# Kernel tuning notes

Hardware: AMD Instinct MI355X
Metric: run time of the kernel (lower is better)

Reference implementation:

```python
import jax, jax.numpy as jnp
import numpy as np

N = 200000          # nodes
E = 12_800_000      # edges (avg degree 64)
C = 4               # conv_out_channels == node_features
H = 32              # lstm_out_channels


def setup_inputs() -> dict:
    key = jax.random.key(0)
    ks = jax.random.split(key, 16)
    inv_c = 1.0 / np.sqrt(C)
    inv_h = 1.0 / np.sqrt(H)
    return {
        "x": jax.random.normal(ks[0], (N, C), jnp.float32),
        "edge_index": jax.random.randint(ks[1], (2, E), 0, N, dtype=jnp.int64),
        "edge_weight": jax.random.uniform(ks[2], (E,), jnp.float32),
        "h_0": 0.1 * jax.random.normal(ks[3], (1, N, H), jnp.float32),
        "c_0": 0.1 * jax.random.normal(ks[4], (1, N, H), jnp.float32),
        # GatedGraphConv (num_layers=1): weight[0] of shape [C, C]
        "conv_weight": inv_c * jax.random.normal(ks[5], (C, C), jnp.float32),
        # GRUCell(C, C) params (PyTorch layout: [3C, C], gate order r,z,n)
        "gru_w_ih": inv_c * jax.random.normal(ks[6], (3 * C, C), jnp.float32),
        "gru_w_hh": inv_c * jax.random.normal(ks[7], (3 * C, C), jnp.float32),
        "gru_b_ih": inv_c * jax.random.normal(ks[8], (3 * C,), jnp.float32),
        "gru_b_hh": inv_c * jax.random.normal(ks[9], (3 * C,), jnp.float32),
        # LSTM(C, H, 1 layer) params (PyTorch layout: [4H, *], gate order i,f,g,o)
        "lstm_w_ih": inv_h * jax.random.normal(ks[10], (4 * H, C), jnp.float32),
        "lstm_w_hh": inv_h * jax.random.normal(ks[11], (4 * H, H), jnp.float32),
        "lstm_b_ih": inv_h * jax.random.normal(ks[12], (4 * H,), jnp.float32),
        "lstm_b_hh": inv_h * jax.random.normal(ks[13], (4 * H,), jnp.float32),
        # Linear(32, 1)
        "lin_w": inv_h * jax.random.normal(ks[14], (1, H), jnp.float32),
        "lin_b": inv_h * jax.random.normal(ks[15], (1,), jnp.float32),
    }


def reference(x, edge_index, edge_weight, h_0, c_0,
              conv_weight, gru_w_ih, gru_w_hh, gru_b_ih, gru_b_hh,
              lstm_w_ih, lstm_w_hh, lstm_b_ih, lstm_b_hh, lin_w, lin_b):
    n = x.shape[0]
    src, dst = edge_index[0], edge_index[1]  # source j -> target i

    # ---- GatedGraphConv, 1 layer (in_dim == out_channels, no padding) ----
    m = x @ conv_weight                                   # [N, C]
    msg = m[src] * edge_weight[:, None]                   # [E, C] gather
    summed = jax.ops.segment_sum(msg, dst, num_segments=n)
    cnt = jax.ops.segment_sum(jnp.ones((msg.shape[0],), msg.dtype), dst,
                              num_segments=n)
    agg = summed / jnp.maximum(cnt, 1.0)[:, None]         # mean aggr (empty -> 0)

    # GRUCell(agg, x): r,z,n gate order
    gi = agg @ gru_w_ih.T + gru_b_ih
    gh = x @ gru_w_hh.T + gru_b_hh
    i_r, i_z, i_n = jnp.split(gi, 3, axis=1)
    h_r, h_z, h_n = jnp.split(gh, 3, axis=1)
    r = jax.nn.sigmoid(i_r + h_r)
    z = jax.nn.sigmoid(i_z + h_z)
    nn_ = jnp.tanh(i_n + r * h_n)
    h_conv = (1.0 - z) * nn_ + z * x                      # [N, C]

    # ---- LSTM: seq_len=1, batch=N, 1 layer; gate order i,f,g,o ----
    h_prev, c_prev = h_0[0], c_0[0]                       # [N, H]
    gates = h_conv @ lstm_w_ih.T + lstm_b_ih + h_prev @ lstm_w_hh.T + lstm_b_hh
    ig, fg, gg, og = jnp.split(gates, 4, axis=1)
    ig, fg, og = jax.nn.sigmoid(ig), jax.nn.sigmoid(fg), jax.nn.sigmoid(og)
    gg = jnp.tanh(gg)
    c_new = fg * c_prev + ig * gg
    h_new = og * jnp.tanh(c_new)                          # [N, H]

    # ---- relu + linear head ----
    out = jax.nn.relu(h_new) @ lin_w.T + lin_b            # [N, 1]
    return out, h_new[None], c_new[None]
```

## Files before the change

### kernel.cpp

```cpp
#include <hip/hip_runtime.h>
#include <math.h>

#define B_SHIFT 8
#define BMASK   255
#define CHUNK   8192
#define CITER   (CHUNK / (NTHR * 4))
#define NTHR    256
#define SEG     4

#define LDSADD(p, v) __hip_atomic_fetch_add((p), (v), __ATOMIC_RELAXED, \
                                            __HIP_MEMORY_SCOPE_WORKGROUP)

static __device__ __forceinline__ float sigf(float x) {
  return 1.0f / (1.0f + __expf(-x));
}
static __device__ __forceinline__ float tanhfast(float x) {
  return 2.0f / (1.0f + __expf(-2.0f * x)) - 1.0f;
}

__global__ void conv_m_kernel(const float* __restrict__ x,
                              const float* __restrict__ w,
                              float* __restrict__ m, int n) {
  int i = blockIdx.x * blockDim.x + threadIdx.x;
  if (i >= n) return;
  float4 xv = reinterpret_cast<const float4*>(x)[i];
  float4 mv;
  mv.x = xv.x * w[0] + xv.y * w[4] + xv.z * w[8]  + xv.w * w[12];
  mv.y = xv.x * w[1] + xv.y * w[5] + xv.z * w[9]  + xv.w * w[13];
  mv.z = xv.x * w[2] + xv.y * w[6] + xv.z * w[10] + xv.w * w[14];
  mv.w = xv.x * w[3] + xv.y * w[7] + xv.z * w[11] + xv.w * w[15];
  reinterpret_cast<float4*>(m)[i] = mv;
}


__global__ __launch_bounds__(NTHR) void hist_kernel(const int* __restrict__ dst,
                                                    int E, int B,
                                                    int* __restrict__ gCnt) {
  __shared__ int h[1024];
  for (int b = threadIdx.x; b < B; b += NTHR) h[b] = 0;
  __syncthreads();
  const int4* d4 = reinterpret_cast<const int4*>(dst);
  int i4base = (int)(((long long)blockIdx.x * CHUNK) >> 2);
  int lim4 = E >> 2;
#pragma unroll
  for (int j = 0; j < CITER; ++j) {
    int i4 = i4base + j * NTHR + threadIdx.x;
    if (i4 < lim4) {
      int4 d = d4[i4];
      atomicAdd(&h[d.x >> B_SHIFT], 1);
      atomicAdd(&h[d.y >> B_SHIFT], 1);
      atomicAdd(&h[d.z >> B_SHIFT], 1);
      atomicAdd(&h[d.w >> B_SHIFT], 1);
    }
  }
  if (blockIdx.x == 0 && threadIdx.x == 0) {
    for (int e = E & ~3; e < E; ++e) atomicAdd(&h[dst[e] >> B_SHIFT], 1);
  }
  __syncthreads();
  for (int b = threadIdx.x; b < B; b += NTHR) {
    int c = h[b];
    if (c) atomicAdd(&gCnt[b], c);
  }
}

__global__ void scan_kernel(const int* __restrict__ gCnt, int B,
                            int* __restrict__ start, int* __restrict__ cursor) {
  __shared__ int s[1024];
  int t = threadIdx.x;
  int v = (t < B) ? gCnt[t] : 0;
  s[t] = v;
  __syncthreads();
  for (int off = 1; off < 1024; off <<= 1) {
    int u = (t >= off) ? s[t - off] : 0;
    __syncthreads();
    s[t] += u;
    __syncthreads();
  }
  if (t < B) {
    int excl = (t == 0) ? 0 : s[t - 1];
    start[t] = excl;
    cursor[t] = excl;
  }
  if (t == 0) start[B] = s[1023];
}

__global__ __launch_bounds__(NTHR) void bin_kernel(const int* __restrict__ ei,
                                                   const float* __restrict__ ew,
                                                   int E, int B,
                                                   int* __restrict__ cursor,
                                                   int2* __restrict__ binned) {
  __shared__ int h[1024];
  for (int b = threadIdx.x; b < B; b += NTHR) h[b] = 0;
  __syncthreads();
  const int* dst = ei + E;
  const int4* d4 = reinterpret_cast<const int4*>(dst);
  const int4* s4 = reinterpret_cast<const int4*>(ei);
  const float4* w4 = reinterpret_cast<const float4*>(ew);
  int i4base = (int)(((long long)blockIdx.x * CHUNK) >> 2);
  int lim4 = E >> 2;
#pragma unroll
  for (int j = 0; j < CITER; ++j) {
    int i4 = i4base + j * NTHR + threadIdx.x;
    if (i4 < lim4) {
      int4 d = d4[i4];
      atomicAdd(&h[d.x >> B_SHIFT], 1);
      atomicAdd(&h[d.y >> B_SHIFT], 1);
      atomicAdd(&h[d.z >> B_SHIFT], 1);
      atomicAdd(&h[d.w >> B_SHIFT], 1);
    }
  }
  __syncthreads();
  for (int b = threadIdx.x; b < B; b += NTHR) {
    int c = h[b];
    if (c) h[b] = atomicAdd(&cursor[b], c);
  }
  __syncthreads();
#pragma unroll
  for (int j = 0; j < CITER; ++j) {
    int i4 = i4base + j * NTHR + threadIdx.x;
    if (i4 < lim4) {
      int4 d = d4[i4];
      int4 s = s4[i4];
      float4 w = w4[i4];
      int p;
      p = atomicAdd(&h[d.x >> B_SHIFT], 1);
      binned[p] = make_int2((s.x << B_SHIFT) | (d.x & BMASK), __float_as_int(w.x));
      p = atomicAdd(&h[d.y >> B_SHIFT], 1);
      binned[p] = make_int2((s.y << B_SHIFT) | (d.y & BMASK), __float_as_int(w.y));
      p = atomicAdd(&h[d.z >> B_SHIFT], 1);
      binned[p] = make_int2((s.z << B_SHIFT) | (d.z & BMASK), __float_as_int(w.z));
      p = atomicAdd(&h[d.w >> B_SHIFT], 1);
      binned[p] = make_int2((s.w << B_SHIFT) | (d.w & BMASK), __float_as_int(w.w));
    }
  }
  if (blockIdx.x == 0 && threadIdx.x == 0) {
    for (int e = E & ~3; e < E; ++e) {
      int d = dst[e];
      int p = atomicAdd(&cursor[d >> B_SHIFT], 1);
      binned[p] = make_int2((ei[e] << B_SHIFT) | (d & BMASK), __float_as_int(ew[e]));
    }
  }
}

__global__ __launch_bounds__(NTHR) void edge_agg_kernel(
    const float* __restrict__ m, const int2* __restrict__ binned,
    const int* __restrict__ start, float* __restrict__ sumBuf,
    float* __restrict__ cntBuf, int n) {
  __shared__ float acc[NTHR * 5];
  int tid = threadIdx.x;
  int b = blockIdx.x;
#pragma unroll
  for (int k = 0; k < 5; ++k) acc[k * NTHR + tid] = 0.0f;
  __syncthreads();

  int s0 = start[b], e0 = start[b + 1];
  int len = e0 - s0;
  int s = s0 + (int)((long long)len * blockIdx.y / SEG);
  int e = s0 + (int)((long long)len * (blockIdx.y + 1) / SEG);

  const float4* m4 = reinterpret_cast<const float4*>(m);
  int i = s + tid;
  for (; i + 7 * NTHR < e; i += 8 * NTHR) {
    int2 r[8];
    float4 v[8];
#pragma unroll
    for (int u = 0; u < 8; ++u) r[u] = binned[i + u * NTHR];
#pragma unroll
    for (int u = 0; u < 8; ++u) v[u] = m4[r[u].x >> B_SHIFT];
#pragma unroll
    for (int u = 0; u < 8; ++u) {
      float w = __int_as_float(r[u].y);
      int a = (r[u].x & BMASK) * 5;
      LDSADD(&acc[a + 0], v[u].x * w);
      LDSADD(&acc[a + 1], v[u].y * w);
      LDSADD(&acc[a + 2], v[u].z * w);
      LDSADD(&acc[a + 3], v[u].w * w);
      LDSADD(&acc[a + 4], 1.0f);
    }
  }
  for (; i < e; i += NTHR) {
    int2 r = binned[i];
    float4 v = m4[r.x >> B_SHIFT];
    float w = __int_as_float(r.y);
    int a = (r.x & BMASK) * 5;
    LDSADD(&acc[a + 0], v.x * w);
    LDSADD(&acc[a + 1], v.y * w);
    LDSADD(&acc[a + 2], v.z * w);
    LDSADD(&acc[a + 3], v.w * w);
    LDSADD(&acc[a + 4], 1.0f);
  }
  __syncthreads();

  int node = (b << B_SHIFT) + tid;
  if (node < n) {
    float c = acc[tid * 5 + 4];
    if (c != 0.0f) {
      unsafeAtomicAdd(&sumBuf[(size_t)node * 4 + 0], acc[tid * 5 + 0]);
      unsafeAtomicAdd(&sumBuf[(size_t)node * 4 + 1], acc[tid * 5 + 1]);
      unsafeAtomicAdd(&sumBuf[(size_t)node * 4 + 2], acc[tid * 5 + 2]);
      unsafeAtomicAdd(&sumBuf[(size_t)node * 4 + 3], acc[tid * 5 + 3]);
      unsafeAtomicAdd(&cntBuf[node], c);
    }
  }
}

__global__ __launch_bounds__(NTHR) void node_kernel2(
    const float* __restrict__ x, const float* __restrict__ sumBuf,
    const float* __restrict__ cntBuf,
    const float* __restrict__ h0, const float* __restrict__ c0,
    const float* __restrict__ gwi, const float* __restrict__ gwh,
    const float* __restrict__ gbi, const float* __restrict__ gbh,
    const float* __restrict__ lwi, const float* __restrict__ lwh,
    const float* __restrict__ lbi, const float* __restrict__ lbh,
    const float* __restrict__ linw, const float* __restrict__ linb,
    float* __restrict__ out, float* __restrict__ hout, float* __restrict__ cout,
    int n) {
  __shared__ float4 s_lwh[1024];
  __shared__ float4 s_lwi[128];
  __shared__ float  s_lb[128];
  __shared__ float  s_linw[32];
  __shared__ float  s_gwi[48], s_gwh[48], s_gbi[12], s_gbh[12];

  int tid = threadIdx.x;
  for (int k = tid; k < 4096; k += NTHR) ((float*)s_lwh)[k] = lwh[k];
  for (int k = tid; k < 512; k += NTHR) ((float*)s_lwi)[k] = lwi[k];
  if (tid < 128) s_lb[tid] = lbi[tid] + lbh[tid];
  if (tid < 32) s_linw[tid] = linw[tid];
  if (tid < 48) { s_gwi[tid] = gwi[tid]; s_gwh[tid] = gwh[tid]; }
  if (tid < 12) { s_gbi[tid] = gbi[tid]; s_gbh[tid] = gbh[tid]; }
  __syncthreads();

  int i = blockIdx.x * blockDim.x + tid;
  if (i >= n) return;

  float4 sv = reinterpret_cast<const float4*>(sumBuf)[i];
  float inv = 1.0f / fmaxf(cntBuf[i], 1.0f);
  float agg[4] = {sv.x * inv, sv.y * inv, sv.z * inv, sv.w * inv};
  float4 xv = reinterpret_cast<const float4*>(x)[i];
  float xa[4] = {xv.x, xv.y, xv.z, xv.w};

  float hc[4];
#pragma unroll
  for (int c = 0; c < 4; ++c) {
    float gi_r = s_gbi[c],     gh_r = s_gbh[c];
    float gi_z = s_gbi[4 + c], gh_z = s_gbh[4 + c];
    float gi_n = s_gbi[8 + c], gh_n = s_gbh[8 + c];
#pragma unroll
    for (int k = 0; k < 4; ++k) {
      gi_r += agg[k] * s_gwi[c * 4 + k];       gh_r += xa[k] * s_gwh[c * 4 + k];
      gi_z += agg[k] * s_gwi[(4 + c) * 4 + k]; gh_z += xa[k] * s_gwh[(4 + c) * 4 + k];
      gi_n += agg[k] * s_gwi[(8 + c) * 4 + k]; gh_n += xa[k] * s_gwh[(8 + c) * 4 + k];
    }
    float r = sigf(gi_r + gh_r);
    float z = sigf(gi_z + gh_z);
    float nn = tanhfast(gi_n + r * gh_n);
    hc[c] = (1.0f - z) * nn + z * xa[c];
  }

  const float4* h04 = reinterpret_cast<const float4*>(h0) + (size_t)i * 8;
  const float4* c04 = reinterpret_cast<const float4*>(c0) + (size_t)i * 8;
  float hp[32];
#pragma unroll
  for (int q = 0; q < 8; ++q) {
    float4 hv = h04[q];
    hp[q * 4 + 0] = hv.x; hp[q * 4 + 1] = hv.y;
    hp[q * 4 + 2] = hv.z; hp[q * 4 + 3] = hv.w;
  }
  float oacc = linb[0];
  float4* hout4 = reinterpret_cast<float4*>(hout) + (size_t)i * 8;
  float4* cout4 = reinterpret_cast<float4*>(cout) + (size_t)i * 8;

#pragma unroll
  for (int jc = 0; jc < 8; ++jc) {
    float4 cpv = c04[jc];
    float cpa[4] = {cpv.x, cpv.y, cpv.z, cpv.w};
    float hn[4], cn[4];
#pragma unroll
    for (int jj = 0; jj < 4; ++jj) {
      int j = jc * 4 + jj;
      float gI = s_lb[j];
      float gF = s_lb[32 + j];
      float gG = s_lb[64 + j];
      float gO = s_lb[96 + j];
      float4 wi = s_lwi[j], wf = s_lwi[32 + j], wg = s_lwi[64 + j], wo = s_lwi[96 + j];
      gI += hc[0] * wi.x + hc[1] * wi.y + hc[2] * wi.z + hc[3] * wi.w;
      gF += hc[0] * wf.x + hc[1] * wf.y + hc[2] * wf.z + hc[3] * wf.w;
      gG += hc[0] * wg.x + hc[1] * wg.y + hc[2] * wg.z + hc[3] * wg.w;
      gO += hc[0] * wo.x + hc[1] * wo.y + hc[2] * wo.z + hc[3] * wo.w;
#pragma unroll
      for (int q = 0; q < 8; ++q) {
        float4 a = s_lwh[j * 8 + q];
        float4 b = s_lwh[(32 + j) * 8 + q];
        float4 g = s_lwh[(64 + j) * 8 + q];
        float4 o = s_lwh[(96 + j) * 8 + q];
        float p0 = hp[q * 4 + 0], p1 = hp[q * 4 + 1];
        float p2 = hp[q * 4 + 2], p3 = hp[q * 4 + 3];
        gI += p0 * a.x + p1 * a.y + p2 * a.z + p3 * a.w;
        gF += p0 * b.x + p1 * b.y + p2 * b.z + p3 * b.w;
        gG += p0 * g.x + p1 * g.y + p2 * g.z + p3 * g.w;
        gO += p0 * o.x + p1 * o.y + p2 * o.z + p3 * o.w;
      }
      float ig = sigf(gI), fg = sigf(gF), og = sigf(gO), gg = tanhfast(gG);
      float cnew = fg * cpa[jj] + ig * gg;
      float hnew = og * tanhfast(cnew);
      cn[jj] = cnew; hn[jj] = hnew;
      oacc += fmaxf(hnew, 0.0f) * s_linw[j];
    }
    hout4[jc] = make_float4(hn[0], hn[1], hn[2], hn[3]);
    cout4[jc] = make_float4(cn[0], cn[1], cn[2], cn[3]);
  }
  out[i] = oacc;
}


__global__ void edge_kernel(const int* __restrict__ ei,
                            const float* __restrict__ ew,
                            const float* __restrict__ m,
                            float* __restrict__ summed,
                            float* __restrict__ cnt, int E) {
  int t = blockIdx.x * blockDim.x + threadIdx.x;
  int e0 = t * 4;
  const float4* m4 = reinterpret_cast<const float4*>(m);
  for (int e = e0; e < E && e < e0 + 4; ++e) {
    int s = ei[e], d = ei[E + e];
    float w = ew[e];
    float4 mv = m4[s];
    float* p = summed + 4ll * d;
    unsafeAtomicAdd(p + 0, mv.x * w);
    unsafeAtomicAdd(p + 1, mv.y * w);
    unsafeAtomicAdd(p + 2, mv.z * w);
    unsafeAtomicAdd(p + 3, mv.w * w);
    unsafeAtomicAdd(cnt + d, 1.0f);
  }
}

__global__ __launch_bounds__(NTHR) void node_kernel(
    const float* __restrict__ x, const float* __restrict__ summed,
    const float* __restrict__ cnt,
    const float* __restrict__ h0, const float* __restrict__ c0,
    const float* __restrict__ gwi, const float* __restrict__ gwh,
    const float* __restrict__ gbi, const float* __restrict__ gbh,
    const float* __restrict__ lwi, const float* __restrict__ lwh,
    const float* __restrict__ lbi, const float* __restrict__ lbh,
    const float* __restrict__ linw, const float* __restrict__ linb,
    float* __restrict__ out, float* __restrict__ hout, float* __restrict__ cout,
    int n) {
  int i = blockIdx.x * blockDim.x + threadIdx.x;
  if (i >= n) return;
  float4 sv = reinterpret_cast<const float4*>(summed)[i];
  float inv = 1.0f / fmaxf(cnt[i], 1.0f);
  float agg[4] = {sv.x * inv, sv.y * inv, sv.z * inv, sv.w * inv};
  float4 xv = reinterpret_cast<const float4*>(x)[i];
  float xa[4] = {xv.x, xv.y, xv.z, xv.w};
  float hc[4];
#pragma unroll
  for (int c = 0; c < 4; ++c) {
    float gi_r = gbi[c],     gh_r = gbh[c];
    float gi_z = gbi[4 + c], gh_z = gbh[4 + c];
    float gi_n = gbi[8 + c], gh_n = gbh[8 + c];
#pragma unroll
    for (int k = 0; k < 4; ++k) {
      gi_r += agg[k] * gwi[c * 4 + k];       gh_r += xa[k] * gwh[c * 4 + k];
      gi_z += agg[k] * gwi[(4 + c) * 4 + k]; gh_z += xa[k] * gwh[(4 + c) * 4 + k];
      gi_n += agg[k] * gwi[(8 + c) * 4 + k]; gh_n += xa[k] * gwh[(8 + c) * 4 + k];
    }
    float r = sigf(gi_r + gh_r);
    float z = sigf(gi_z + gh_z);
    float nn = tanhfast(gi_n + r * gh_n);
    hc[c] = (1.0f - z) * nn + z * xa[c];
  }
  const float4* h04 = reinterpret_cast<const float4*>(h0) + (size_t)i * 8;
  const float4* c04 = reinterpret_cast<const float4*>(c0) + (size_t)i * 8;
  float hp[32];
#pragma unroll
  for (int q = 0; q < 8; ++q) {
    float4 hv = h04[q];
    hp[q * 4 + 0] = hv.x; hp[q * 4 + 1] = hv.y;
    hp[q * 4 + 2] = hv.z; hp[q * 4 + 3] = hv.w;
  }
  const float4* wih4 = reinterpret_cast<const float4*>(lwi);
  const float4* whh4 = reinterpret_cast<const float4*>(lwh);
  float oacc = linb[0];
  float4* hout4 = reinterpret_cast<float4*>(hout) + (size_t)i * 8;
  float4* cout4 = reinterpret_cast<float4*>(cout) + (size_t)i * 8;
#pragma unroll
  for (int jc = 0; jc < 8; ++jc) {
    float4 cpv = c04[jc];
    float cpa[4] = {cpv.x, cpv.y, cpv.z, cpv.w};
    float hn[4], cn[4];
#pragma unroll
    for (int jj = 0; jj < 4; ++jj) {
      int j = jc * 4 + jj;
      float gI = lbi[j]      + lbh[j];
      float gF = lbi[32 + j] + lbh[32 + j];
      float gG = lbi[64 + j] + lbh[64 + j];
      float gO = lbi[96 + j] + lbh[96 + j];
      float4 wi = wih4[j], wf = wih4[32 + j], wg = wih4[64 + j], wo = wih4[96 + j];
      gI += hc[0] * wi.x + hc[1] * wi.y + hc[2] * wi.z + hc[3] * wi.w;
      gF += hc[0] * wf.x + hc[1] * wf.y + hc[2] * wf.z + hc[3] * wf.w;
      gG += hc[0] * wg.x + hc[1] * wg.y + hc[2] * wg.z + hc[3] * wg.w;
      gO += hc[0] * wo.x + hc[1] * wo.y + hc[2] * wo.z + hc[3] * wo.w;
#pragma unroll
      for (int q = 0; q < 8; ++q) {
        float4 a = whh4[j * 8 + q];
        float4 b = whh4[(32 + j) * 8 + q];
        float4 g = whh4[(64 + j) * 8 + q];
        float4 o = whh4[(96 + j) * 8 + q];
        float p0 = hp[q * 4 + 0], p1 = hp[q * 4 + 1];
        float p2 = hp[q * 4 + 2], p3 = hp[q * 4 + 3];
        gI += p0 * a.x + p1 * a.y + p2 * a.z + p3 * a.w;
        gF += p0 * b.x + p1 * b.y + p2 * b.z + p3 * b.w;
        gG += p0 * g.x + p1 * g.y + p2 * g.z + p3 * g.w;
        gO += p0 * o.x + p1 * o.y + p2 * o.z + p3 * o.w;
      }
      float ig = sigf(gI), fg = sigf(gF), og = sigf(gO), gg = tanhfast(gG);
      float cnew = fg * cpa[jj] + ig * gg;
      float hnew = og * tanhfast(cnew);
      cn[jj] = cnew; hn[jj] = hnew;
      oacc += fmaxf(hnew, 0.0f) * linw[j];
    }
    hout4[jc] = make_float4(hn[0], hn[1], hn[2], hn[3]);
    cout4[jc] = make_float4(cn[0], cn[1], cn[2], cn[3]);
  }
  out[i] = oacc;
}

extern "C" void kernel_launch(void* const* d_in, const int* in_sizes, int n_in,
                              void* d_out, int out_size, void* d_ws, size_t ws_size,
                              hipStream_t stream) {
  const float* x     = (const float*)d_in[0];
  const int*   ei    = (const int*)d_in[1];
  const float* ew    = (const float*)d_in[2];
  const float* h0    = (const float*)d_in[3];
  const float* c0    = (const float*)d_in[4];
  const float* convw = (const float*)d_in[5];
  const float* gwi   = (const float*)d_in[6];
  const float* gwh   = (const float*)d_in[7];
  const float* gbi   = (const float*)d_in[8];
  const float* gbh   = (const float*)d_in[9];
  const float* lwi   = (const float*)d_in[10];
  const float* lwh   = (const float*)d_in[11];
  const float* lbi   = (const float*)d_in[12];
  const float* lbh   = (const float*)d_in[13];
  const float* linw  = (const float*)d_in[14];
  const float* linb  = (const float*)d_in[15];

  int n = in_sizes[0] / 4;
  int E = in_sizes[1] / 2;

  float* out  = (float*)d_out;
  float* hout = out + n;
  float* cout = hout + (size_t)n * 32;

  int B = (n + BMASK) >> B_SHIFT;
  size_t need = (size_t)E * 8 + (size_t)n * 36 + ((size_t)3 * B + 2) * 4 + 64;

  if (B <= 1024 && ws_size >= need) {
    int2*  binned = (int2*)d_ws;
    float* m      = (float*)(binned + E);
    float* sumBuf = m + (size_t)n * 4;
    float* cntBuf = sumBuf + (size_t)n * 4;
    int*   gCnt   = (int*)(cntBuf + n);
    int*   start  = gCnt + B;
    int*   cursor = start + B + 1;

    hipMemsetAsync(gCnt, 0, (size_t)B * sizeof(int), stream);
    hipMemsetAsync(sumBuf, 0, (size_t)n * 5 * sizeof(float), stream);
    conv_m_kernel<<<(n + NTHR - 1) / NTHR, NTHR, 0, stream>>>(x, convw, m, n);

    int nbBlocks = (E + CHUNK - 1) / CHUNK;
    hist_kernel<<<nbBlocks, NTHR, 0, stream>>>(ei + E, E, B, gCnt);
    scan_kernel<<<1, 1024, 0, stream>>>(gCnt, B, start, cursor);
    bin_kernel<<<nbBlocks, NTHR, 0, stream>>>(ei, ew, E, B, cursor, binned);

    edge_agg_kernel<<<dim3(B, SEG), NTHR, 0, stream>>>(m, binned, start,
                                                       sumBuf, cntBuf, n);
    node_kernel2<<<(n + NTHR - 1) / NTHR, NTHR, 0, stream>>>(
        x, sumBuf, cntBuf, h0, c0,
        gwi, gwh, gbi, gbh, lwi, lwh, lbi, lbh, linw, linb,
        out, hout, cout, n);
  } else {
    float* m      = (float*)d_ws;
    float* summed = m + (size_t)n * 4;
    float* cntp   = summed + (size_t)n * 4;
    hipMemsetAsync(summed, 0, (size_t)n * 5 * sizeof(float), stream);
    conv_m_kernel<<<(n + NTHR - 1) / NTHR, NTHR, 0, stream>>>(x, convw, m, n);
    int et = (E + 3) / 4;
    edge_kernel<<<(et + NTHR - 1) / NTHR, NTHR, 0, stream>>>(ei, ew, m, summed, cntp, E);
    node_kernel<<<(n + NTHR - 1) / NTHR, NTHR, 0, stream>>>(
        x, summed, cntp, h0, c0,
        gwi, gwh, gbi, gbh, lwi, lwh, lbi, lbh, linw, linb,
        out, hout, cout, n);
  }
}
```

Measured before the change: 955.8 us.

## Replace bucketed edge binning with per-node CSR build and fused gather aggregation

Instead of binning edges into 256-node buckets with LDS atomics and a separate aggregation kernel, builds a full per-node CSR: global atomic histogram of destinations, a three-stage scan, and an atomic-cursor scatter. The node kernel then gathers each node's edges directly and computes the mean before the GRU/LSTM, fusing the aggregation and dropping the sum/count buffers and their memset. The cost is 12.8M global atomics on per-node counters, done twice, plus a thread-per-node gather loop that is uncoalesced and diverges with node degree.

```diff
diff --git a/kernel.cpp b/kernel.cpp
--- a/kernel.cpp
+++ b/kernel.cpp
@@ -1,15 +1,8 @@
 #include <hip/hip_runtime.h>
 #include <math.h>
 
-#define B_SHIFT 8
-#define BMASK   255
-#define CHUNK   8192
-#define CITER   (CHUNK / (NTHR * 4))
-#define NTHR    256
-#define SEG     4
-
-#define LDSADD(p, v) __hip_atomic_fetch_add((p), (v), __ATOMIC_RELAXED, \
-                                            __HIP_MEMORY_SCOPE_WORKGROUP)
+#define NTHR  256
+#define SCTH  1024
 
 static __device__ __forceinline__ float sigf(float x) {
   return 1.0f / (1.0f + __expf(-x));
@@ -33,180 +26,97 @@
 }
 
 
-__global__ __launch_bounds__(NTHR) void hist_kernel(const int* __restrict__ dst,
-                                                    int E, int B,
-                                                    int* __restrict__ gCnt) {
-  __shared__ int h[1024];
-  for (int b = threadIdx.x; b < B; b += NTHR) h[b] = 0;
-  __syncthreads();
-  const int4* d4 = reinterpret_cast<const int4*>(dst);
-  int i4base = (int)(((long long)blockIdx.x * CHUNK) >> 2);
+__global__ __launch_bounds__(NTHR) void nodehist_kernel(
+    const int* __restrict__ dst, int E, int* __restrict__ nodeCnt) {
+  int i4 = blockIdx.x * blockDim.x + threadIdx.x;
   int lim4 = E >> 2;
-#pragma unroll
-  for (int j = 0; j < CITER; ++j) {
-    int i4 = i4base + j * NTHR + threadIdx.x;
-    if (i4 < lim4) {
-      int4 d = d4[i4];
-      atomicAdd(&h[d.x >> B_SHIFT], 1);
-      atomicAdd(&h[d.y >> B_SHIFT], 1);
-      atomicAdd(&h[d.z >> B_SHIFT], 1);
-      atomicAdd(&h[d.w >> B_SHIFT], 1);
-    }
-  }
-  if (blockIdx.x == 0 && threadIdx.x == 0) {
-    for (int e = E & ~3; e < E; ++e) atomicAdd(&h[dst[e] >> B_SHIFT], 1);
-  }
-  __syncthreads();
-  for (int b = threadIdx.x; b < B; b += NTHR) {
-    int c = h[b];
-    if (c) atomicAdd(&gCnt[b], c);
-  }
-}
-
-__global__ void scan_kernel(const int* __restrict__ gCnt, int B,
-                            int* __restrict__ start, int* __restrict__ cursor) {
-  __shared__ int s[1024];
-  int t = threadIdx.x;
-  int v = (t < B) ? gCnt[t] : 0;
+  if (i4 < lim4) {
+    int4 d = reinterpret_cast<const int4*>(dst)[i4];
+    atomicAdd(&nodeCnt[d.x], 1);
+    atomicAdd(&nodeCnt[d.y], 1);
+    atomicAdd(&nodeCnt[d.z], 1);
+    atomicAdd(&nodeCnt[d.w], 1);
+  }
+  if (i4 == 0) {
+    for (int e = E & ~3; e < E; ++e) atomicAdd(&nodeCnt[dst[e]], 1);
+  }
+}
+
+__global__ void scan1_kernel(const int* __restrict__ in, int n,
+                             int* __restrict__ outExcl,
+                             int* __restrict__ blockSum) {
+  __shared__ int s[SCTH];
+  int t = threadIdx.x, g = blockIdx.x * SCTH + t;
+  int v = (g < n) ? in[g] : 0;
   s[t] = v;
   __syncthreads();
-  for (int off = 1; off < 1024; off <<= 1) {
+  for (int off = 1; off < SCTH; off <<= 1) {
     int u = (t >= off) ? s[t - off] : 0;
     __syncthreads();
     s[t] += u;
     __syncthreads();
   }
-  if (t < B) {
-    int excl = (t == 0) ? 0 : s[t - 1];
-    start[t] = excl;
-    cursor[t] = excl;
-  }
-  if (t == 0) start[B] = s[1023];
-}
-
-__global__ __launch_bounds__(NTHR) void bin_kernel(const int* __restrict__ ei,
-                                                   const float* __restrict__ ew,
-                                                   int E, int B,
-                                                   int* __restrict__ cursor,
-                                                   int2* __restrict__ binned) {
-  __shared__ int h[1024];
-  for (int b = threadIdx.x; b < B; b += NTHR) h[b] = 0;
+  if (g < n) outExcl[g] = s[t] - v;
+  if (t == SCTH - 1) blockSum[blockIdx.x] = s[t];
+}
+
+__global__ void scan2_kernel(const int* __restrict__ blockSum, int nb,
+                             int* __restrict__ blockOff) {
+  __shared__ int s[SCTH];
+  int t = threadIdx.x;
+  int v = (t < nb) ? blockSum[t] : 0;
+  s[t] = v;
   __syncthreads();
-  const int* dst = ei + E;
-  const int4* d4 = reinterpret_cast<const int4*>(dst);
-  const int4* s4 = reinterpret_cast<const int4*>(ei);
-  const float4* w4 = reinterpret_cast<const float4*>(ew);
-  int i4base = (int)(((long long)blockIdx.x * CHUNK) >> 2);
+  for (int off = 1; off < SCTH; off <<= 1) {
+    int u = (t >= off) ? s[t - off] : 0;
+    __syncthreads();
+    s[t] += u;
+    __syncthreads();
+  }
+  if (t < nb) blockOff[t] = s[t] - v;
+}
+
+__global__ void scan3_kernel(int* __restrict__ nodeStart,
+                             int* __restrict__ nodeCursor,
+                             const int* __restrict__ blockOff, int n) {
+  int g = blockIdx.x * SCTH + threadIdx.x;
+  if (g < n) {
+    int v = nodeStart[g] + blockOff[blockIdx.x];
+    nodeStart[g] = v;
+    nodeCursor[g] = v;
+  }
+}
+
+__global__ __launch_bounds__(NTHR) void csr_scatter_kernel(
+    const int* __restrict__ ei, const float* __restrict__ ew, int E,
+    int* __restrict__ nodeCursor, int2* __restrict__ csr) {
+  int i4 = blockIdx.x * blockDim.x + threadIdx.x;
   int lim4 = E >> 2;
-#pragma unroll
-  for (int j = 0; j < CITER; ++j) {
-    int i4 = i4base + j * NTHR + threadIdx.x;
-    if (i4 < lim4) {
-      int4 d = d4[i4];
-      atomicAdd(&h[d.x >> B_SHIFT], 1);
-      atomicAdd(&h[d.y >> B_SHIFT], 1);
-      atomicAdd(&h[d.z >> B_SHIFT], 1);
-      atomicAdd(&h[d.w >> B_SHIFT], 1);
+  if (i4 < lim4) {
+    int4 s = reinterpret_cast<const int4*>(ei)[i4];
+    int4 d = reinterpret_cast<const int4*>(ei + E)[i4];
+    float4 w = reinterpret_cast<const float4*>(ew)[i4];
+    int p0 = atomicAdd(&nodeCursor[d.x], 1);
+    int p1 = atomicAdd(&nodeCursor[d.y], 1);
+    int p2 = atomicAdd(&nodeCursor[d.z], 1);
+    int p3 = atomicAdd(&nodeCursor[d.w], 1);
+    csr[p0] = make_int2(s.x, __float_as_int(w.x));
+    csr[p1] = make_int2(s.y, __float_as_int(w.y));
+    csr[p2] = make_int2(s.z, __float_as_int(w.z));
+    csr[p3] = make_int2(s.w, __float_as_int(w.w));
+  }
+  if (i4 == 0) {
+    for (int e = E & ~3; e < E; ++e) {
+      int p = atomicAdd(&nodeCursor[ei[E + e]], 1);
+      csr[p] = make_int2(ei[e], __float_as_int(ew[e]));
     }
   }
-  __syncthreads();
-  for (int b = threadIdx.x; b < B; b += NTHR) {
-    int c = h[b];
-    if (c) h[b] = atomicAdd(&cursor[b], c);
-  }
-  __syncthreads();
-#pragma unroll
-  for (int j = 0; j < CITER; ++j) {
-    int i4 = i4base + j * NTHR + threadIdx.x;
-    if (i4 < lim4) {
-      int4 d = d4[i4];
-      int4 s = s4[i4];
-      float4 w = w4[i4];
-      int p;
-      p = atomicAdd(&h[d.x >> B_SHIFT], 1);
-      binned[p] = make_int2((s.x << B_SHIFT) | (d.x & BMASK), __float_as_int(w.x));
-      p = atomicAdd(&h[d.y >> B_SHIFT], 1);
-      binned[p] = make_int2((s.y << B_SHIFT) | (d.y & BMASK), __float_as_int(w.y));
-      p = atomicAdd(&h[d.z >> B_SHIFT], 1);
-      binned[p] = make_int2((s.z << B_SHIFT) | (d.z & BMASK), __float_as_int(w.z));
-      p = atomicAdd(&h[d.w >> B_SHIFT], 1);
-      binned[p] = make_int2((s.w << B_SHIFT) | (d.w & BMASK), __float_as_int(w.w));
-    }
-  }
-  if (blockIdx.x == 0 && threadIdx.x == 0) {
-    for (int e = E & ~3; e < E; ++e) {
-      int d = dst[e];
-      int p = atomicAdd(&cursor[d >> B_SHIFT], 1);
-      binned[p] = make_int2((ei[e] << B_SHIFT) | (d & BMASK), __float_as_int(ew[e]));
-    }
-  }
-}
-
-__global__ __launch_bounds__(NTHR) void edge_agg_kernel(
-    const float* __restrict__ m, const int2* __restrict__ binned,
-    const int* __restrict__ start, float* __restrict__ sumBuf,
-    float* __restrict__ cntBuf, int n) {
-  __shared__ float acc[NTHR * 5];
-  int tid = threadIdx.x;
-  int b = blockIdx.x;
-#pragma unroll
-  for (int k = 0; k < 5; ++k) acc[k * NTHR + tid] = 0.0f;
-  __syncthreads();
-
-  int s0 = start[b], e0 = start[b + 1];
-  int len = e0 - s0;
-  int s = s0 + (int)((long long)len * blockIdx.y / SEG);
-  int e = s0 + (int)((long long)len * (blockIdx.y + 1) / SEG);
-
-  const float4* m4 = reinterpret_cast<const float4*>(m);
-  int i = s + tid;
-  for (; i + 7 * NTHR < e; i += 8 * NTHR) {
-    int2 r[8];
-    float4 v[8];
-#pragma unroll
-    for (int u = 0; u < 8; ++u) r[u] = binned[i + u * NTHR];
-#pragma unroll
-    for (int u = 0; u < 8; ++u) v[u] = m4[r[u].x >> B_SHIFT];
-#pragma unroll
-    for (int u = 0; u < 8; ++u) {
-      float w = __int_as_float(r[u].y);
-      int a = (r[u].x & BMASK) * 5;
-      LDSADD(&acc[a + 0], v[u].x * w);
-      LDSADD(&acc[a + 1], v[u].y * w);
-      LDSADD(&acc[a + 2], v[u].z * w);
-      LDSADD(&acc[a + 3], v[u].w * w);
-      LDSADD(&acc[a + 4], 1.0f);
-    }
-  }
-  for (; i < e; i += NTHR) {
-    int2 r = binned[i];
-    float4 v = m4[r.x >> B_SHIFT];
-    float w = __int_as_float(r.y);
-    int a = (r.x & BMASK) * 5;
-    LDSADD(&acc[a + 0], v.x * w);
-    LDSADD(&acc[a + 1], v.y * w);
-    LDSADD(&acc[a + 2], v.z * w);
-    LDSADD(&acc[a + 3], v.w * w);
-    LDSADD(&acc[a + 4], 1.0f);
-  }
-  __syncthreads();
-
-  int node = (b << B_SHIFT) + tid;
-  if (node < n) {
-    float c = acc[tid * 5 + 4];
-    if (c != 0.0f) {
-      unsafeAtomicAdd(&sumBuf[(size_t)node * 4 + 0], acc[tid * 5 + 0]);
-      unsafeAtomicAdd(&sumBuf[(size_t)node * 4 + 1], acc[tid * 5 + 1]);
-      unsafeAtomicAdd(&sumBuf[(size_t)node * 4 + 2], acc[tid * 5 + 2]);
-      unsafeAtomicAdd(&sumBuf[(size_t)node * 4 + 3], acc[tid * 5 + 3]);
-      unsafeAtomicAdd(&cntBuf[node], c);
-    }
-  }
-}
-
-__global__ __launch_bounds__(NTHR) void node_kernel2(
-    const float* __restrict__ x, const float* __restrict__ sumBuf,
-    const float* __restrict__ cntBuf,
+}
+
+__global__ __launch_bounds__(NTHR) void agg_gru_lstm_kernel(
+    const float* __restrict__ x, const float* __restrict__ m,
+    const int2* __restrict__ csr, const int* __restrict__ nodeStart,
+    const int* __restrict__ nodeCnt,
     const float* __restrict__ h0, const float* __restrict__ c0,
     const float* __restrict__ gwi, const float* __restrict__ gwh,
     const float* __restrict__ gbi, const float* __restrict__ gbh,
@@ -233,9 +143,33 @@
   int i = blockIdx.x * blockDim.x + tid;
   if (i >= n) return;
 
-  float4 sv = reinterpret_cast<const float4*>(sumBuf)[i];
-  float inv = 1.0f / fmaxf(cntBuf[i], 1.0f);
-  float agg[4] = {sv.x * inv, sv.y * inv, sv.z * inv, sv.w * inv};
+  const float4* m4 = reinterpret_cast<const float4*>(m);
+  int p = nodeStart[i];
+  int cnt = nodeCnt[i];
+  int e = p + cnt;
+  float ax = 0.0f, ay = 0.0f, az = 0.0f, aw = 0.0f;
+  for (; p + 4 <= e; p += 4) {
+    int2 r0 = csr[p], r1 = csr[p + 1], r2 = csr[p + 2], r3 = csr[p + 3];
+    float4 v0 = m4[r0.x];
+    float4 v1 = m4[r1.x];
+    float4 v2 = m4[r2.x];
+    float4 v3 = m4[r3.x];
+    float w0 = __int_as_float(r0.y), w1 = __int_as_float(r1.y);
+    float w2 = __int_as_float(r2.y), w3 = __int_as_float(r3.y);
+    ax += v0.x * w0 + v1.x * w1 + v2.x * w2 + v3.x * w3;
+    ay += v0.y * w0 + v1.y * w1 + v2.y * w2 + v3.y * w3;
+    az += v0.z * w0 + v1.z * w1 + v2.z * w2 + v3.z * w3;
+    aw += v0.w * w0 + v1.w * w1 + v2.w * w2 + v3.w * w3;
+  }
+  for (; p < e; ++p) {
+    int2 r = csr[p];
+    float4 v = m4[r.x];
+    float w = __int_as_float(r.y);
+    ax += v.x * w; ay += v.y * w; az += v.z * w; aw += v.w * w;
+  }
+  float inv = 1.0f / fmaxf((float)cnt, 1.0f);
+  float agg[4] = {ax * inv, ay * inv, az * inv, aw * inv};
+
   float4 xv = reinterpret_cast<const float4*>(x)[i];
   float xa[4] = {xv.x, xv.y, xv.z, xv.w};
 
@@ -452,31 +386,32 @@
   float* hout = out + n;
   float* cout = hout + (size_t)n * 32;
 
-  int B = (n + BMASK) >> B_SHIFT;
-  size_t need = (size_t)E * 8 + (size_t)n * 36 + ((size_t)3 * B + 2) * 4 + 64;
-
-  if (B <= 1024 && ws_size >= need) {
-    int2*  binned = (int2*)d_ws;
-    float* m      = (float*)(binned + E);
-    float* sumBuf = m + (size_t)n * 4;
-    float* cntBuf = sumBuf + (size_t)n * 4;
-    int*   gCnt   = (int*)(cntBuf + n);
-    int*   start  = gCnt + B;
-    int*   cursor = start + B + 1;
-
-    hipMemsetAsync(gCnt, 0, (size_t)B * sizeof(int), stream);
-    hipMemsetAsync(sumBuf, 0, (size_t)n * 5 * sizeof(float), stream);
+  int nbScan = (n + SCTH - 1) / SCTH;
+  size_t need = (size_t)E * 8 + (size_t)n * 16 + (size_t)n * 12 +
+                (size_t)SCTH * 8 + 256;
+
+  if (nbScan <= SCTH && ws_size >= need) {
+    int2*  csr      = (int2*)d_ws;
+    float* m        = (float*)(csr + E);
+    int*   nodeCnt  = (int*)(m + (size_t)n * 4);
+    int*   nodeSt   = nodeCnt + n;
+    int*   nodeCur  = nodeSt + n;
+    int*   blockSum = nodeCur + n;
+    int*   blockOff = blockSum + SCTH;
+
+    hipMemsetAsync(nodeCnt, 0, (size_t)n * sizeof(int), stream);
     conv_m_kernel<<<(n + NTHR - 1) / NTHR, NTHR, 0, stream>>>(x, convw, m, n);
 
-    int nbBlocks = (E + CHUNK - 1) / CHUNK;
-    hist_kernel<<<nbBlocks, NTHR, 0, stream>>>(ei + E, E, B, gCnt);
-    scan_kernel<<<1, 1024, 0, stream>>>(gCnt, B, start, cursor);
-    bin_kernel<<<nbBlocks, NTHR, 0, stream>>>(ei, ew, E, B, cursor, binned);
-
-    edge_agg_kernel<<<dim3(B, SEG), NTHR, 0, stream>>>(m, binned, start,
-                                                       sumBuf, cntBuf, n);
-    node_kernel2<<<(n + NTHR - 1) / NTHR, NTHR, 0, stream>>>(
-        x, sumBuf, cntBuf, h0, c0,
+    int e4 = E >> 2;
+    int ehBlocks = (e4 + NTHR - 1) / NTHR;
+    nodehist_kernel<<<ehBlocks, NTHR, 0, stream>>>(ei + E, E, nodeCnt);
+    scan1_kernel<<<nbScan, SCTH, 0, stream>>>(nodeCnt, n, nodeSt, blockSum);
+    scan2_kernel<<<1, SCTH, 0, stream>>>(blockSum, nbScan, blockOff);
+    scan3_kernel<<<nbScan, SCTH, 0, stream>>>(nodeSt, nodeCur, blockOff, n);
+    csr_scatter_kernel<<<ehBlocks, NTHR, 0, stream>>>(ei, ew, E, nodeCur, csr);
+
+    agg_gru_lstm_kernel<<<(n + NTHR - 1) / NTHR, NTHR, 0, stream>>>(
+        x, m, csr, nodeSt, nodeCnt, h0, c0,
         gwi, gwh, gbi, gbh, lwi, lwh, lbi, lbh, linw, linb,
         out, hout, cout, n);
   } else {
```

New measurement: 1.962 ms. 2.05x slower.
